# Kernel optimization log

Hardware: AMD Instinct MI355X
Metric: run time of the kernel (lower is better)

## Reference

```python
import jax, jax.numpy as jnp
import numpy as np
from jax import lax

B, N_SITES, FEAT, BOND, OUT = 2048, 128, 64, 32, 256
CORE_SCALE = 0.02  # keeps the 128-step matrix product finite


def setup_inputs() -> dict:
    key = jax.random.key(0)
    ks = jax.random.split(key, 6)
    return {
        "x": jax.random.normal(ks[0], (B, N_SITES, FEAT), dtype=jnp.float32),
        "cores": jax.random.normal(ks[1], (N_SITES, BOND, FEAT, BOND), dtype=jnp.float32) * CORE_SCALE,
        "start": jax.random.normal(ks[2], (1, BOND), dtype=jnp.float32),
        "end": jax.random.normal(ks[3], (BOND, 1), dtype=jnp.float32),
        "fc_w": jax.random.normal(ks[4], (OUT, 1), dtype=jnp.float32),
        "fc_b": jax.random.normal(ks[5], (OUT,), dtype=jnp.float32),
    }


def reference(x, cores, start, end, fc_w, fc_b):
    # x: [B, N, F]; cores: [N, D, F, D]; start: [1, D]; end: [D, 1]
    b = x.shape[0]
    res0 = jnp.broadcast_to(start, (b, start.shape[1]))  # [B, D]

    def step(res, site):
        xi, core = site  # xi: [B, F], core: [D, F, D]
        m = jnp.einsum('bf,dfr->bdr', xi, core)  # per-site transfer matrix [B, D, D]
        return jnp.einsum('bd,bdr->br', res, m), None

    res, _ = lax.scan(step, res0, (jnp.swapaxes(x, 0, 1), cores))
    val = res @ end  # [B, 1]
    return val @ fc_w.T + fc_b  # [B, OUT]
```

## Files before the change

kernel.cpp:

```cpp
#include <hip/hip_runtime.h>


#define NSITES 128
#define FEATD  64
#define BOND   32
#define OUTD   256
#define BT     16
#define SEGLEN 16
#define NSEG   (NSITES / SEGLEN)
#define NBT    (2048 / BT)

#define RSTRIDE 48
#define BSTRIDE 1552

typedef __attribute__((ext_vector_type(4))) float float4v;

__device__ __forceinline__ unsigned pk4_fp8(float a, float b, float c, float d) {
    int v = __builtin_amdgcn_cvt_pk_fp8_f32(a, b, 0, false);
    v = __builtin_amdgcn_cvt_pk_fp8_f32(c, d, v, true);
    return (unsigned)v;
}

__global__ __launch_bounds__(256)
void prep_cores8(const float* __restrict__ cores, unsigned char* __restrict__ core8) {
    __shared__ float tile[FEATD][BOND + 4];
    const int nd = blockIdx.x;
    const int t  = threadIdx.x;
    const float* src = cores + (size_t)nd * (FEATD * BOND);
    {
        int base = t * 8;
        int f = base >> 5, r0 = base & 31;
        float4 v0 = *(const float4*)(src + base);
        float4 v1 = *(const float4*)(src + base + 4);
        tile[f][r0 + 0] = v0.x; tile[f][r0 + 1] = v0.y;
        tile[f][r0 + 2] = v0.z; tile[f][r0 + 3] = v0.w;
        tile[f][r0 + 4] = v1.x; tile[f][r0 + 5] = v1.y;
        tile[f][r0 + 6] = v1.z; tile[f][r0 + 7] = v1.w;
    }
    __syncthreads();
    const int r = t >> 3, f0 = (t & 7) * 8;
    const float s = 16.0f;
    unsigned lo = pk4_fp8(tile[f0 + 0][r] * s, tile[f0 + 1][r] * s,
                          tile[f0 + 2][r] * s, tile[f0 + 3][r] * s);
    unsigned hi = pk4_fp8(tile[f0 + 4][r] * s, tile[f0 + 5][r] * s,
                          tile[f0 + 6][r] * s, tile[f0 + 7][r] * s);
    uint2 w; w.x = lo; w.y = hi;
    *(uint2*)(core8 + ((size_t)nd * BOND + r) * FEATD + f0) = w;
}

__global__ __launch_bounds__(512, 8)
void mps_seg(const float* __restrict__ x, const unsigned char* __restrict__ core8,
             unsigned char* __restrict__ Pout) {
    __shared__ __align__(16) unsigned char MS[BT * BSTRIDE];
    __shared__ __align__(16) unsigned char XS[BT * 72];

    const int t    = threadIdx.x;
    const int wave = t >> 6;
    const int lane = t & 63;
    const int cl   = lane & 15;
    const int q    = lane >> 4;
    const int b0   = blockIdx.x * BT;
    const int seg  = blockIdx.y;

    int pw[2][2][2];
#pragma unroll
    for (int bi = 0; bi < 2; ++bi)
#pragma unroll
        for (int I = 0; I < 2; ++I)
#pragma unroll
            for (int J = 0; J < 2; ++J) {
                int v = 0;
                int g = cl - 4 * q;
                if (I == J && g >= 0 && g < 4) v = 0x58 << (g * 8);
                pw[bi][I][J] = v;
            }

    const int xb = t >> 5, xf = (t & 31) * 2;
    float2 xf2 = *(const float2*)(x + ((size_t)(b0 + xb) * NSITES + seg * SEGLEN) * FEATD + xf);
    {
        int v = __builtin_amdgcn_cvt_pk_fp8_f32(xf2.x, xf2.y, 0, false);
        *(unsigned short*)&XS[xb * 72 + xf] = (unsigned short)(v & 0xffff);
    }

    const int hi32  = (lane & 32) ? 1 : 0;
    const int addr0 = (cl + ((lane & 16) << 1)) * 4;
    const int addr1 = addr0 + 64;

    for (int k = 0; k < SEGLEN; ++k) {
        const int n = seg * SEGLEN + k;
        __syncthreads();

        const unsigned char* cbase = core8 + (size_t)n * (1024 * FEATD);
        long bx0 = *(const long*)&XS[cl * 72 + q * 8];
        long bx1 = *(const long*)&XS[cl * 72 + 32 + q * 8];

        float2 xn;
        if (k + 1 < SEGLEN)
            xn = *(const float2*)(x + ((size_t)(b0 + xb) * NSITES + n + 1) * FEATD + xf);

#pragma unroll
        for (int p = 0; p < 2; ++p) {
            long afA[4], afB[4];
#pragma unroll
            for (int u = 0; u < 4; ++u) {
                const unsigned char* ptr =
                    cbase + (size_t)((wave * 8 + 2 * u + p) * 16 + cl) * FEATD + q * 8;
                afA[u] = *(const long*)ptr;
                afB[u] = *(const long*)(ptr + 32);
            }
            float4v acc[4];
#pragma unroll
            for (int u = 0; u < 4; ++u) {
                float4v z = {0.f, 0.f, 0.f, 0.f};
                z = __builtin_amdgcn_mfma_f32_16x16x32_fp8_fp8(afA[u], bx0, z, 0, 0, 0);
                acc[u] = __builtin_amdgcn_mfma_f32_16x16x32_fp8_fp8(afB[u], bx1, z, 0, 0, 0);
            }
#pragma unroll
            for (int g = 0; g < 4; ++g) {
                unsigned w = pk4_fp8(acc[0][g], acc[1][g], acc[2][g], acc[3][g]);
                *(unsigned*)&MS[cl * BSTRIDE + (16 * p + 4 * q + g) * RSTRIDE + wave * 4] = w;
            }
        }

        __syncthreads();

#pragma unroll
        for (int bi = 0; bi < 2; ++bi) {
            const int bb = wave * 2 + bi;
            long pa0 = *(const long*)&MS[bb * BSTRIDE + (0 * 16 + cl) * RSTRIDE + q * 8];
            long pa1 = *(const long*)&MS[bb * BSTRIDE + (1 * 16 + cl) * RSTRIDE + q * 8];
            long pbv[2];
#pragma unroll
            for (int h = 0; h < 2; ++h) {
                int l0a = __builtin_amdgcn_ds_bpermute(addr0, pw[bi][0][h]);
                int l0b = __builtin_amdgcn_ds_bpermute(addr0, pw[bi][1][h]);
                int l1a = __builtin_amdgcn_ds_bpermute(addr1, pw[bi][0][h]);
                int l1b = __builtin_amdgcn_ds_bpermute(addr1, pw[bi][1][h]);
                int d0 = hi32 ? l0b : l0a;
                int d1 = hi32 ? l1b : l1a;
                pbv[h] = ((long)(unsigned)d0) | (((long)d1) << 32);
            }
            float4v pc[2][2];
#pragma unroll
            for (int I = 0; I < 2; ++I)
#pragma unroll
                for (int J = 0; J < 2; ++J) {
                    float4v z = {0.f, 0.f, 0.f, 0.f};
                    pc[I][J] = __builtin_amdgcn_mfma_f32_16x16x32_fp8_fp8(
                        I ? pa1 : pa0, pbv[J], z, 0, 0, 0);
                }
#pragma unroll
            for (int I = 0; I < 2; ++I)
#pragma unroll
                for (int J = 0; J < 2; ++J)
                    pw[bi][I][J] = (int)pk4_fp8(pc[I][J][0] * 0.0625f, pc[I][J][1] * 0.0625f,
                                                pc[I][J][2] * 0.0625f, pc[I][J][3] * 0.0625f);
        }

        if (k + 1 < SEGLEN) {
            int v = __builtin_amdgcn_cvt_pk_fp8_f32(xn.x, xn.y, 0, false);
            *(unsigned short*)&XS[xb * 72 + xf] = (unsigned short)(v & 0xffff);
        }
    }

#pragma unroll
    for (int bi = 0; bi < 2; ++bi) {
        const int bb = wave * 2 + bi;
        unsigned char* gp = Pout + (((size_t)seg * 2048 + b0 + bb) * 1024);
#pragma unroll
        for (int I = 0; I < 2; ++I)
#pragma unroll
            for (int J = 0; J < 2; ++J)
                *(unsigned*)(gp + (J * 16 + cl) * 32 + I * 16 + q * 4) =
                    (unsigned)pw[bi][I][J];
    }
}

__global__ __launch_bounds__(512)
void combine(const unsigned char* __restrict__ Pout, const float* __restrict__ startv,
             const float* __restrict__ endv, const float* __restrict__ fc_w,
             const float* __restrict__ fc_b, float* __restrict__ out) {
    const int t    = threadIdx.x;
    const int wave = t >> 6;
    const int lane = t & 63;
    const int r    = lane >> 1;
    const int dh   = lane & 1;
    const int b    = blockIdx.x * 8 + wave;

    float res = startv[r];
    const unsigned char* base = Pout + (size_t)b * 1024 + dh * 512 + r;

    unsigned char by[16];
#pragma unroll
    for (int di = 0; di < 16; ++di) by[di] = base[di * 32];

    for (int s = 0; s < NSEG; ++s) {
        unsigned char by2[16];
        if (s + 1 < NSEG) {
            const unsigned char* nb = base + (size_t)(s + 1) * 2048 * 1024;
#pragma unroll
            for (int di = 0; di < 16; ++di) by2[di] = nb[di * 32];
        }
        float acc = 0.f;
#pragma unroll
        for (int di = 0; di < 16; ++di) {
            float rv = __shfl(res, dh * 32 + di * 2, 64);
            acc += rv * __builtin_amdgcn_cvt_f32_fp8((int)by[di], 0);
        }
        float tot = acc + __shfl_xor(acc, 1, 64);
        res = tot * 0.0625f;
        if (s + 1 < NSEG) {
#pragma unroll
            for (int di = 0; di < 16; ++di) by[di] = by2[di];
        }
    }

    float v = dh ? 0.f : res * endv[r];
#pragma unroll
    for (int off = 1; off < 64; off <<= 1) v += __shfl_xor(v, off, 64);

    const int j = lane * 4;
    float4 w4  = *(const float4*)(fc_w + j);
    float4 bb4 = *(const float4*)(fc_b + j);
    float4 o;
    o.x = v * w4.x + bb4.x;
    o.y = v * w4.y + bb4.y;
    o.z = v * w4.z + bb4.z;
    o.w = v * w4.w + bb4.w;
    *(float4*)(out + (size_t)b * OUTD + j) = o;
}

extern "C" void kernel_launch(void* const* d_in, const int* in_sizes, int n_in,
                              void* d_out, int out_size, void* d_ws, size_t ws_size,
                              hipStream_t stream) {
    const float* x      = (const float*)d_in[0];
    const float* cores  = (const float*)d_in[1];
    const float* startv = (const float*)d_in[2];
    const float* endv   = (const float*)d_in[3];
    const float* fc_w   = (const float*)d_in[4];
    const float* fc_b   = (const float*)d_in[5];
    float* out = (float*)d_out;

    unsigned char* core8 = (unsigned char*)d_ws;
    unsigned char* Pout  = core8 + (size_t)NSITES * 1024 * FEATD;

    prep_cores8<<<NSITES * BOND, 256, 0, stream>>>(cores, core8);
    mps_seg<<<dim3(NBT, NSEG), 512, 0, stream>>>(x, core8, Pout);
    combine<<<2048 / 8, 512, 0, stream>>>(Pout, startv, endv, fc_w, fc_b, out);
}
```

Baseline: 266.1 us.

## Double batch tile and segment length, keep core fragments in registers with prefetch

Doubles the batch tile to 32 and the segment length to 32, launching 1024-thread blocks where two wave groups share the same core fragments. Core fragments are now held in registers and the next site's fragments are prefetched after the barrier, so the global load overlaps the chain-product step. The final segment products are staged through shared memory for wide coalesced stores. The trade-offs are higher register pressure, fewer blocks per CU, and longer sequential chains per block, which cut parallelism across segments.

Measured after the change: 268.7 us. No clear change (+1.0%).

```diff
diff --git a/kernel.cpp b/kernel.cpp
--- a/kernel.cpp
+++ b/kernel.cpp
@@ -5,8 +5,8 @@
 #define FEATD  64
 #define BOND   32
 #define OUTD   256
-#define BT     16
-#define SEGLEN 16
+#define BT     32
+#define SEGLEN 32
 #define NSEG   (NSITES / SEGLEN)
 #define NBT    (2048 / BT)
 
@@ -48,7 +48,7 @@
     *(uint2*)(core8 + ((size_t)nd * BOND + r) * FEATD + f0) = w;
 }
 
-__global__ __launch_bounds__(512, 8)
+__global__ __launch_bounds__(1024, 4)
 void mps_seg(const float* __restrict__ x, const unsigned char* __restrict__ core8,
              unsigned char* __restrict__ Pout) {
     __shared__ __align__(16) unsigned char MS[BT * BSTRIDE];
@@ -59,6 +59,8 @@
     const int lane = t & 63;
     const int cl   = lane & 15;
     const int q    = lane >> 4;
+    const int cb   = wave & 7;
+    const int bh   = wave >> 3;
     const int b0   = blockIdx.x * BT;
     const int seg  = blockIdx.y;
 
@@ -75,54 +77,61 @@
                 pw[bi][I][J] = v;
             }
 
-    const int xb = t >> 5, xf = (t & 31) * 2;
-    float2 xf2 = *(const float2*)(x + ((size_t)(b0 + xb) * NSITES + seg * SEGLEN) * FEATD + xf);
-    {
-        int v = __builtin_amdgcn_cvt_pk_fp8_f32(xf2.x, xf2.y, 0, false);
-        *(unsigned short*)&XS[xb * 72 + xf] = (unsigned short)(v & 0xffff);
-    }
-
     const int hi32  = (lane & 32) ? 1 : 0;
     const int addr0 = (cl + ((lane & 16) << 1)) * 4;
     const int addr1 = addr0 + 64;
 
+    const int xb = t >> 5, xf = (t & 31) * 2;
+    const unsigned afoff = (unsigned)((cb * 8 * 16 + cl) * FEATD + q * 8);
+
+    {
+        float2 x0 = *(const float2*)(x + ((size_t)(b0 + xb) * NSITES + seg * SEGLEN) * FEATD + xf);
+        int v = __builtin_amdgcn_cvt_pk_fp8_f32(x0.x, x0.y, 0, false);
+        *(unsigned short*)&XS[xb * 72 + xf] = (unsigned short)(v & 0xffff);
+    }
+    long af[16];
+    {
+        const unsigned char* p0 = core8 + (size_t)(seg * SEGLEN) * (1024 * FEATD) + afoff;
+#pragma unroll
+        for (int i = 0; i < 8; ++i) {
+            af[i * 2 + 0] = *(const long*)(p0 + i * (16 * FEATD));
+            af[i * 2 + 1] = *(const long*)(p0 + i * (16 * FEATD) + 32);
+        }
+    }
+
     for (int k = 0; k < SEGLEN; ++k) {
         const int n = seg * SEGLEN + k;
         __syncthreads();
 
-        const unsigned char* cbase = core8 + (size_t)n * (1024 * FEATD);
-        long bx0 = *(const long*)&XS[cl * 72 + q * 8];
-        long bx1 = *(const long*)&XS[cl * 72 + 32 + q * 8];
+        long bx0 = *(const long*)&XS[(bh * 16 + cl) * 72 + q * 8];
+        long bx1 = *(const long*)&XS[(bh * 16 + cl) * 72 + 32 + q * 8];
+        float4v acc[8];
+#pragma unroll
+        for (int i = 0; i < 8; ++i) {
+            float4v z = {0.f, 0.f, 0.f, 0.f};
+            z = __builtin_amdgcn_mfma_f32_16x16x32_fp8_fp8(af[i * 2 + 0], bx0, z, 0, 0, 0);
+            acc[i] = __builtin_amdgcn_mfma_f32_16x16x32_fp8_fp8(af[i * 2 + 1], bx1, z, 0, 0, 0);
+        }
+#pragma unroll
+        for (int p = 0; p < 2; ++p)
+#pragma unroll
+            for (int g = 0; g < 4; ++g) {
+                unsigned w = pk4_fp8(acc[p][g], acc[p + 2][g], acc[p + 4][g], acc[p + 6][g]);
+                *(unsigned*)&MS[(bh * 16 + cl) * BSTRIDE + (16 * p + 4 * q + g) * RSTRIDE + cb * 4] = w;
+            }
+
+        __syncthreads();
 
         float2 xn;
-        if (k + 1 < SEGLEN)
+        if (k + 1 < SEGLEN) {
             xn = *(const float2*)(x + ((size_t)(b0 + xb) * NSITES + n + 1) * FEATD + xf);
-
-#pragma unroll
-        for (int p = 0; p < 2; ++p) {
-            long afA[4], afB[4];
-#pragma unroll
-            for (int u = 0; u < 4; ++u) {
-                const unsigned char* ptr =
-                    cbase + (size_t)((wave * 8 + 2 * u + p) * 16 + cl) * FEATD + q * 8;
-                afA[u] = *(const long*)ptr;
-                afB[u] = *(const long*)(ptr + 32);
-            }
-            float4v acc[4];
-#pragma unroll
-            for (int u = 0; u < 4; ++u) {
-                float4v z = {0.f, 0.f, 0.f, 0.f};
-                z = __builtin_amdgcn_mfma_f32_16x16x32_fp8_fp8(afA[u], bx0, z, 0, 0, 0);
-                acc[u] = __builtin_amdgcn_mfma_f32_16x16x32_fp8_fp8(afB[u], bx1, z, 0, 0, 0);
-            }
-#pragma unroll
-            for (int g = 0; g < 4; ++g) {
-                unsigned w = pk4_fp8(acc[0][g], acc[1][g], acc[2][g], acc[3][g]);
-                *(unsigned*)&MS[cl * BSTRIDE + (16 * p + 4 * q + g) * RSTRIDE + wave * 4] = w;
-            }
-        }
-
-        __syncthreads();
+            const unsigned char* p1 = core8 + (size_t)(n + 1) * (1024 * FEATD) + afoff;
+#pragma unroll
+            for (int i = 0; i < 8; ++i) {
+                af[i * 2 + 0] = *(const long*)(p1 + i * (16 * FEATD));
+                af[i * 2 + 1] = *(const long*)(p1 + i * (16 * FEATD) + 32);
+            }
+        }
 
 #pragma unroll
         for (int bi = 0; bi < 2; ++bi) {
@@ -163,16 +172,26 @@
         }
     }
 
+    __syncthreads();
 #pragma unroll
     for (int bi = 0; bi < 2; ++bi) {
         const int bb = wave * 2 + bi;
-        unsigned char* gp = Pout + (((size_t)seg * 2048 + b0 + bb) * 1024);
 #pragma unroll
         for (int I = 0; I < 2; ++I)
 #pragma unroll
             for (int J = 0; J < 2; ++J)
-                *(unsigned*)(gp + (J * 16 + cl) * 32 + I * 16 + q * 4) =
+                *(unsigned*)&MS[bb * 1024 + (J * 16 + cl) * 32 + I * 16 + q * 4] =
                     (unsigned)pw[bi][I][J];
+    }
+    __syncthreads();
+    {
+        int b = t >> 5, chunk = t & 31;
+        const uint4* p = (const uint4*)&MS[b * 1024 + chunk * 32];
+        uint4 v0 = p[0];
+        uint4 v1 = p[1];
+        uint4* g = (uint4*)(Pout + (((size_t)seg * 2048 + b0 + b) * 1024 + chunk * 32));
+        g[0] = v0;
+        g[1] = v1;
     }
 }
 
@@ -245,6 +264,6 @@
     unsigned char* Pout  = core8 + (size_t)NSITES * 1024 * FEATD;
 
     prep_cores8<<<NSITES * BOND, 256, 0, stream>>>(cores, core8);
-    mps_seg<<<dim3(NBT, NSEG), 512, 0, stream>>>(x, core8, Pout);
+    mps_seg<<<dim3(NBT, NSEG), 1024, 0, stream>>>(x, core8, Pout);
     combine<<<2048 / 8, 512, 0, stream>>>(Pout, startv, endv, fc_w, fc_b, out);
 }
```
